# Kernel optimization log

Hardware: AMD Instinct MI355X
Metric: run time of the kernel (lower is better)

## Reference

```python
import jax, jax.numpy as jnp
import numpy as np

SENSORS = 50000
X_DIM = 64
HID = 64
Y_DIM = 32
N_EDGES = 800000


def setup_inputs() -> dict:
    key = jax.random.key(0)
    k0, k1, k2, k3 = jax.random.split(key, 4)
    x_input = jax.random.normal(k0, (1, X_DIM, SENSORS), dtype=jnp.float32)
    edge_index = jax.random.randint(k1, (2, N_EDGES), 0, SENSORS, dtype=jnp.int32)
    # GCNConv parameters (glorot-ish scaling)
    W1 = jax.random.normal(k2, (X_DIM, HID), dtype=jnp.float32) / np.sqrt(X_DIM)
    b1 = jnp.zeros((HID,), dtype=jnp.float32)
    W2 = jax.random.normal(k3, (HID, Y_DIM), dtype=jnp.float32) / np.sqrt(HID)
    b2 = jnp.zeros((Y_DIM,), dtype=jnp.float32)
    return {"x_input": x_input, "W1": W1, "b1": b1, "W2": W2, "b2": b2,
            "edge_index": edge_index}


def _gcn_conv(x, W, b, src, dst, n_nodes):
    """PyG GCNConv: x' = D^{-1/2}(A+I)D^{-1/2} (x W) + b."""
    h = x @ W  # [N, F_out]
    loop = jnp.arange(n_nodes, dtype=src.dtype)
    s = jnp.concatenate([src, loop])  # add self-loops
    d = jnp.concatenate([dst, loop])
    deg = jax.ops.segment_sum(jnp.ones_like(d, dtype=h.dtype), d,
                              num_segments=n_nodes)
    dinv = jnp.where(deg > 0, jax.lax.rsqrt(deg), 0.0)
    norm = dinv[s] * dinv[d]  # [E+N]
    msg = h[s] * norm[:, None]  # gather source features, scale
    out = jax.ops.segment_sum(msg, d, num_segments=n_nodes)  # scatter-add to targets
    return out + b


def reference(x_input, W1, b1, W2, b2, edge_index):
    B = x_input.shape[0]
    # [B, x, S] -> [B, S, x] -> [B*S, x]
    h = jnp.transpose(x_input, (0, 2, 1)).reshape(-1, X_DIM)
    n_nodes = h.shape[0]
    src, dst = edge_index[0], edge_index[1]
    h = _gcn_conv(h, W1, b1, src, dst, n_nodes)
    h = jax.nn.relu(h)
    h = _gcn_conv(h, W2, b2, src, dst, n_nodes)
    # [B*S, y] -> [B, S, y] -> [B, y, S]
    return jnp.transpose(h.reshape(B, SENSORS, Y_DIM), (0, 2, 1))
```

## Files before the change

kernel.cpp:

```cpp
#include <hip/hip_runtime.h>

#define NS 50000
#define NE 800000
#define XD 64
#define HD 64
#define YD 32

#define SHIFT 7
#define BNODES 128
#define NBUCK 391
#define BCAP 2560
#define NBLKA 256
#define EPB (NE / NBLKA)
#define SCAP 32

__device__ __forceinline__ unsigned f2b(float f) {
    union { float f; unsigned u; } c; c.f = f;
    return (c.u + 0x7fffu + ((c.u >> 16) & 1u)) >> 16;
}
__device__ __forceinline__ float blo(unsigned u) {
    union { unsigned u; float f; } c; c.u = u << 16; return c.f;
}
__device__ __forceinline__ float bhi(unsigned u) {
    union { unsigned u; float f; } c; c.u = u & 0xffff0000u; return c.f;
}

__global__ __launch_bounds__(256) void k_bucket(const int* __restrict__ src,
                                                const int* __restrict__ dst,
                                                int* __restrict__ cnt2,
                                                unsigned* __restrict__ ebuf2) {
    __shared__ unsigned se[EPB];
    __shared__ unsigned short lp[EPB];
    __shared__ int hist[NBUCK];
    int t = threadIdx.x, blk = blockIdx.x;
    int lo = blk * EPB;
    for (int i = t; i < NBUCK; i += 256) hist[i] = 0;
    __syncthreads();
    for (int i = t; i < EPB; i += 256) {
        unsigned d = (unsigned)__builtin_nontemporal_load(dst + lo + i);
        unsigned s = (unsigned)__builtin_nontemporal_load(src + lo + i);
        se[i] = (d << 16) | s;
        lp[i] = (unsigned short)atomicAdd(&hist[d >> SHIFT], 1);
    }
    __syncthreads();
    for (int i = t; i < NBUCK; i += 256)
        cnt2[blk * NBUCK + i] = min(hist[i], SCAP);
    for (int i = t; i < EPB; i += 256) {
        unsigned p = se[i];
        int b = p >> (16 + SHIFT);
        int pos = lp[i];
        if (pos < SCAP)
            ebuf2[((size_t)b * NBLKA + blk) * SCAP + pos] = p;
    }
}

__global__ __launch_bounds__(256) void k_sortxw1(const unsigned* __restrict__ ebuf2,
                                                 const int* __restrict__ cnt2,
                                                 unsigned short* __restrict__ csr,
                                                 int* __restrict__ beg,
                                                 int* __restrict__ endp,
                                                 float* __restrict__ dinv,
                                                 const float* __restrict__ x,
                                                 const float* __restrict__ W1,
                                                 unsigned* __restrict__ G1h) {
    __shared__ float w1[XD * HD];
    __shared__ unsigned se[BCAP];
    __shared__ unsigned short lcsr[BCAP];
    __shared__ int cnt[BNODES];
    __shared__ int offl[BNODES];
    __shared__ int cur[BNODES];
    __shared__ int sm[256];
    __shared__ int wsum[4];
    int b = blockIdx.x, t = threadIdx.x;
    int lane = t & 63, w = t >> 6;
    for (int i = t; i < XD * HD; i += 256) w1[i] = W1[i];
    int c = cnt2[t * NBUCK + b];
    int v = c;
#pragma unroll
    for (int d = 1; d < 64; d <<= 1) {
        int o = __shfl_up(v, d);
        if (lane >= d) v += o;
    }
    if (lane == 63) wsum[w] = v;
    if (t < BNODES) cnt[t] = 0;
    __syncthreads();
    int wpre = 0;
#pragma unroll
    for (int i = 0; i < 4; ++i) wpre += (i < w) ? wsum[i] : 0;
    int soff = wpre + v - c;
    int ntot = wsum[0] + wsum[1] + wsum[2] + wsum[3];
    int n = min(ntot, BCAP);
    {
        const unsigned* sb = ebuf2 + ((size_t)b * NBLKA + t) * SCAP;
        for (int j = 0; j < c; j += 4) {
            uint4 vv = *(const uint4*)&sb[j];
            int p = soff + j;
            if (p < BCAP) se[p] = vv.x;
            if (j + 1 < c && p + 1 < BCAP) se[p + 1] = vv.y;
            if (j + 2 < c && p + 2 < BCAP) se[p + 2] = vv.z;
            if (j + 3 < c && p + 3 < BCAP) se[p + 3] = vv.w;
        }
    }
    __syncthreads();
    for (int i = t; i < n; i += 256) atomicAdd(&cnt[(se[i] >> 16) & (BNODES - 1)], 1);
    __syncthreads();
    int v2 = (t < BNODES) ? cnt[t] : 0;
    sm[t] = v2;
    __syncthreads();
    int val2 = v2;
    for (int o = 1; o < BNODES; o <<= 1) {
        int other = (t >= o) ? sm[t - o] : 0;
        __syncthreads();
        val2 += other;
        sm[t] = val2;
        __syncthreads();
    }
    if (t < BNODES) { offl[t] = val2 - v2; cur[t] = val2 - v2; }
    __syncthreads();
    for (int i = t; i < n; i += 256) {
        unsigned p = se[i];
        int l = (p >> 16) & (BNODES - 1);
        int pos = atomicAdd(&cur[l], 1);
        lcsr[pos] = (unsigned short)(p & 0xffffu);
    }
    __syncthreads();
    unsigned* gc = (unsigned*)(csr + (size_t)b * BCAP);
    int nw = (n + 1) >> 1;
    for (int i = t; i < nw; i += 256) gc[i] = ((const unsigned*)lcsr)[i];
    if (t < BNODES) {
        int node = b * BNODES + t;
        if (node < NS) {
            int bg = b * BCAP + offl[t];
            beg[node] = bg;
            endp[node] = bg + cnt[t];
            dinv[node] = rsqrtf((float)cnt[t] + 1.0f);
        }
    }
    int half = t >> 7, tn = t & (BNODES - 1);
    int node = b * BNODES + tn;
    if (node >= NS) return;
    float4 acc[8];
#pragma unroll
    for (int i = 0; i < 8; ++i) acc[i] = make_float4(0.f, 0.f, 0.f, 0.f);
    for (int xf = 0; xf < XD; ++xf) {
        float xv = __builtin_nontemporal_load(&x[(size_t)xf * NS + node]);
        const float4* wr = (const float4*)&w1[xf * HD + half * 32];
#pragma unroll
        for (int i = 0; i < 8; ++i) {
            float4 wv = wr[i];
            acc[i].x += xv * wv.x; acc[i].y += xv * wv.y;
            acc[i].z += xv * wv.z; acc[i].w += xv * wv.w;
        }
    }
    float dv = rsqrtf((float)cnt[tn] + 1.0f);
    unsigned pk[16];
#pragma unroll
    for (int i = 0; i < 8; ++i) {
        pk[2 * i]     = f2b(dv * acc[i].x) | (f2b(dv * acc[i].y) << 16);
        pk[2 * i + 1] = f2b(dv * acc[i].z) | (f2b(dv * acc[i].w) << 16);
    }
    uint4* o = (uint4*)&G1h[(size_t)node * 32 + half * 16];
#pragma unroll
    for (int i = 0; i < 4; ++i) o[i] = ((uint4*)pk)[i];
}

__global__ __launch_bounds__(256) void k_g1l2(const int* __restrict__ beg,
                                              const int* __restrict__ endp,
                                              const unsigned short* __restrict__ csr,
                                              const unsigned* __restrict__ G1h,
                                              const float* __restrict__ dinv,
                                              const float* __restrict__ b1,
                                              const float* __restrict__ W2,
                                              unsigned* __restrict__ G2h) {
    __shared__ float w2s[HD * YD];
    __shared__ float bsh[HD];
    __shared__ float lds_h[16][68];
    __shared__ float lds_dv[16];
    int t = threadIdx.x;
    for (int i = t; i < HD * YD; i += 256) w2s[i] = W2[i];
    if (t < HD) bsh[t] = b1[t];
    __syncthreads();

    int nl = t >> 4;
    int l  = t & 15;
    int node = blockIdx.x * 16 + nl;
    int beg_ = beg[node], end_ = endp[node];
    float a0 = 0.f, a1 = 0.f, a2 = 0.f, a3 = 0.f;
#pragma unroll 4
    for (int e = beg_; e < end_; ++e) {
        int s = (int)csr[e];
        uint2 u = *(const uint2*)&G1h[(unsigned)s * 32u + 2u * l];
        a0 += blo(u.x); a1 += bhi(u.x);
        a2 += blo(u.y); a3 += bhi(u.y);
    }
    uint2 us = *(const uint2*)&G1h[(unsigned)node * 32u + 2u * l];
    float dv = dinv[node];
    float4 h;
    h.x = fmaxf(fmaf(dv, a0 + blo(us.x), bsh[4 * l + 0]), 0.f);
    h.y = fmaxf(fmaf(dv, a1 + bhi(us.x), bsh[4 * l + 1]), 0.f);
    h.z = fmaxf(fmaf(dv, a2 + blo(us.y), bsh[4 * l + 2]), 0.f);
    h.w = fmaxf(fmaf(dv, a3 + bhi(us.y), bsh[4 * l + 3]), 0.f);
    *(float4*)&lds_h[nl][4 * l] = h;
    if (l == 0) lds_dv[nl] = dv;
    __syncthreads();

    int n2 = t >> 4;
    int oo = (t & 15) * 2;
    float dv2 = lds_dv[n2];
    const float* hr = &lds_h[n2][0];
    float p0 = 0.f, p1 = 0.f;
#pragma unroll
    for (int f4 = 0; f4 < 16; ++f4) {
        float4 hv = *(const float4*)&hr[f4 * 4];
        float2 wa = *(const float2*)&w2s[(f4 * 4 + 0) * YD + oo];
        float2 wb = *(const float2*)&w2s[(f4 * 4 + 1) * YD + oo];
        float2 wc = *(const float2*)&w2s[(f4 * 4 + 2) * YD + oo];
        float2 wd = *(const float2*)&w2s[(f4 * 4 + 3) * YD + oo];
        p0 = fmaf(hv.x, wa.x, p0); p1 = fmaf(hv.x, wa.y, p1);
        p0 = fmaf(hv.y, wb.x, p0); p1 = fmaf(hv.y, wb.y, p1);
        p0 = fmaf(hv.z, wc.x, p0); p1 = fmaf(hv.z, wc.y, p1);
        p0 = fmaf(hv.w, wd.x, p0); p1 = fmaf(hv.w, wd.y, p1);
    }
    int node2 = blockIdx.x * 16 + n2;
    G2h[(size_t)node2 * 16 + (t & 15)] = f2b(dv2 * p0) | (f2b(dv2 * p1) << 16);
}

__global__ __launch_bounds__(256) void k_g2out(const int* __restrict__ beg,
                                               const int* __restrict__ endp,
                                               const unsigned short* __restrict__ csr,
                                               const unsigned* __restrict__ G2h,
                                               const float* __restrict__ dinv,
                                               const float* __restrict__ b2,
                                               float* __restrict__ out) {
    __shared__ float ot[32][33];
    __shared__ float b2s[YD];
    int t = threadIdx.x;
    if (t < YD) b2s[t] = b2[t];
    int g = t >> 3;
    int l = t & 7;
    int base_n = blockIdx.x * 32;
    int node = base_n + g;
    if (node < NS) {
        int beg_ = beg[node], end_ = endp[node];
        float a0 = 0.f, a1 = 0.f, a2 = 0.f, a3 = 0.f;
#pragma unroll 4
        for (int e = beg_; e < end_; ++e) {
            int s = (int)csr[e];
            uint2 u = *(const uint2*)&G2h[(unsigned)s * 16u + 2u * l];
            a0 += blo(u.x); a1 += bhi(u.x);
            a2 += blo(u.y); a3 += bhi(u.y);
        }
        uint2 us = *(const uint2*)&G2h[(unsigned)node * 16u + 2u * l];
        float dv = dinv[node];
        ot[g][4 * l + 0] = dv * (a0 + blo(us.x));
        ot[g][4 * l + 1] = dv * (a1 + bhi(us.x));
        ot[g][4 * l + 2] = dv * (a2 + blo(us.y));
        ot[g][4 * l + 3] = dv * (a3 + bhi(us.y));
    }
    __syncthreads();
#pragma unroll
    for (int k = 0; k < 4; ++k) {
        int idx = k * 256 + t;
        int o = idx >> 5, n = idx & 31;
        int nd = base_n + n;
        if (nd < NS)
            out[(size_t)o * NS + nd] = ot[n][o] + b2s[o];
    }
}

extern "C" void kernel_launch(void* const* d_in, const int* in_sizes, int n_in,
                              void* d_out, int out_size, void* d_ws, size_t ws_size,
                              hipStream_t stream) {
    const float* x  = (const float*)d_in[0];
    const float* W1 = (const float*)d_in[1];
    const float* b1 = (const float*)d_in[2];
    const float* W2 = (const float*)d_in[3];
    const float* b2 = (const float*)d_in[4];
    const int* ei   = (const int*)d_in[5];
    const int* src = ei;
    const int* dst = ei + NE;

    int* cnt2      = (int*)d_ws;
    unsigned* ebuf2 = (unsigned*)(cnt2 + NBLKA * NBUCK);
    unsigned short* csr = (unsigned short*)(ebuf2 + (size_t)NBUCK * NBLKA * SCAP);
    int* beg      = (int*)((unsigned*)csr + (size_t)NBUCK * BCAP / 2);
    int* endp     = beg + 50000;
    float* dinv   = (float*)(endp + 50000);
    unsigned* G1h = (unsigned*)(dinv + 50000);
    unsigned* G2h = G1h + (size_t)50000 * 32;
    float* out    = (float*)d_out;

    k_bucket<<<NBLKA, 256, 0, stream>>>(src, dst, cnt2, ebuf2);
    k_sortxw1<<<NBUCK, 256, 0, stream>>>(ebuf2, cnt2, csr, beg, endp, dinv, x, W1, G1h);
    k_g1l2<<<NS / 16, 256, 0, stream>>>(beg, endp, csr, G1h, dinv, b1, W2, G2h);
    k_g2out<<<(NS + 31) / 32, 256, 0, stream>>>(beg, endp, csr, G2h, dinv, b2, out);
}
```

Baseline: 84.40 us.

## Restructure layer-2 gather as one wavefront per node with in-wave matvec

The fused layer-1 aggregation plus W2 projection kernel now assigns a whole 64-lane wavefront to each node, processed sequentially over four nodes per wave. Each lane gathers one bf16 feature per edge, and the 64x32 matvec is split across the two wave halves and combined with a shuffle. The block-wide barrier between gather and matvec is gone, and the per-lane work is simpler. In exchange, each edge load becomes a 2-byte access, nodes within a wave are serialised, and the code relies on wave-level LDS visibility through __threadfence_block.

New measurement: 99.50 us. +17.9%, slower.

```diff
diff --git a/kernel.cpp b/kernel.cpp
--- a/kernel.cpp
+++ b/kernel.cpp
@@ -23,6 +23,9 @@
 }
 __device__ __forceinline__ float bhi(unsigned u) {
     union { unsigned u; float f; } c; c.u = u & 0xffff0000u; return c.f;
+}
+__device__ __forceinline__ float u2f(unsigned short u) {
+    union { unsigned u; float f; } c; c.u = ((unsigned)u) << 16; return c.f;
 }
 
 __global__ __launch_bounds__(256) void k_bucket(const int* __restrict__ src,
@@ -174,55 +177,41 @@
                                               unsigned* __restrict__ G2h) {
     __shared__ float w2s[HD * YD];
     __shared__ float bsh[HD];
-    __shared__ float lds_h[16][68];
-    __shared__ float lds_dv[16];
+    __shared__ float hrow[4][HD + 4];
     int t = threadIdx.x;
     for (int i = t; i < HD * YD; i += 256) w2s[i] = W2[i];
     if (t < HD) bsh[t] = b1[t];
     __syncthreads();
-
-    int nl = t >> 4;
-    int l  = t & 15;
-    int node = blockIdx.x * 16 + nl;
-    int beg_ = beg[node], end_ = endp[node];
-    float a0 = 0.f, a1 = 0.f, a2 = 0.f, a3 = 0.f;
+    int wv = t >> 6, lane = t & 63;
+    const unsigned short* G1u = (const unsigned short*)G1h;
+    int o = lane & 31, hf = lane >> 5;
+#pragma unroll
+    for (int i = 0; i < 4; ++i) {
+        int node = blockIdx.x * 16 + wv * 4 + i;
+        int beg_ = beg[node], end_ = endp[node];
+        float a = 0.f;
 #pragma unroll 4
-    for (int e = beg_; e < end_; ++e) {
-        int s = (int)csr[e];
-        uint2 u = *(const uint2*)&G1h[(unsigned)s * 32u + 2u * l];
-        a0 += blo(u.x); a1 += bhi(u.x);
-        a2 += blo(u.y); a3 += bhi(u.y);
-    }
-    uint2 us = *(const uint2*)&G1h[(unsigned)node * 32u + 2u * l];
-    float dv = dinv[node];
-    float4 h;
-    h.x = fmaxf(fmaf(dv, a0 + blo(us.x), bsh[4 * l + 0]), 0.f);
-    h.y = fmaxf(fmaf(dv, a1 + bhi(us.x), bsh[4 * l + 1]), 0.f);
-    h.z = fmaxf(fmaf(dv, a2 + blo(us.y), bsh[4 * l + 2]), 0.f);
-    h.w = fmaxf(fmaf(dv, a3 + bhi(us.y), bsh[4 * l + 3]), 0.f);
-    *(float4*)&lds_h[nl][4 * l] = h;
-    if (l == 0) lds_dv[nl] = dv;
-    __syncthreads();
-
-    int n2 = t >> 4;
-    int oo = (t & 15) * 2;
-    float dv2 = lds_dv[n2];
-    const float* hr = &lds_h[n2][0];
-    float p0 = 0.f, p1 = 0.f;
-#pragma unroll
-    for (int f4 = 0; f4 < 16; ++f4) {
-        float4 hv = *(const float4*)&hr[f4 * 4];
-        float2 wa = *(const float2*)&w2s[(f4 * 4 + 0) * YD + oo];
-        float2 wb = *(const float2*)&w2s[(f4 * 4 + 1) * YD + oo];
-        float2 wc = *(const float2*)&w2s[(f4 * 4 + 2) * YD + oo];
-        float2 wd = *(const float2*)&w2s[(f4 * 4 + 3) * YD + oo];
-        p0 = fmaf(hv.x, wa.x, p0); p1 = fmaf(hv.x, wa.y, p1);
-        p0 = fmaf(hv.y, wb.x, p0); p1 = fmaf(hv.y, wb.y, p1);
-        p0 = fmaf(hv.z, wc.x, p0); p1 = fmaf(hv.z, wc.y, p1);
-        p0 = fmaf(hv.w, wd.x, p0); p1 = fmaf(hv.w, wd.y, p1);
-    }
-    int node2 = blockIdx.x * 16 + n2;
-    G2h[(size_t)node2 * 16 + (t & 15)] = f2b(dv2 * p0) | (f2b(dv2 * p1) << 16);
+        for (int e = beg_; e < end_; ++e) {
+            int s = (int)csr[e];
+            a += u2f(G1u[(unsigned)s * 64u + lane]);
+        }
+        float dv = dinv[node];
+        float h = fmaxf(fmaf(dv, a + u2f(G1u[(unsigned)node * 64u + lane]),
+                             bsh[lane]), 0.f);
+        hrow[wv][lane] = h;
+        __threadfence_block();
+        float p = 0.f;
+        const float* hr = &hrow[wv][hf * 32];
+#pragma unroll
+        for (int f = 0; f < 32; ++f)
+            p = fmaf(hr[f], w2s[(hf * 32 + f) * YD + o], p);
+        p += __shfl_xor(p, 32);
+        p *= dv;
+        float pn = __shfl_xor(p, 1);
+        if (hf == 0 && (o & 1) == 0)
+            G2h[(size_t)node * 16 + (o >> 1)] = f2b(p) | (f2b(pn) << 16);
+        __threadfence_block();
+    }
 }
 
 __global__ __launch_bounds__(256) void k_g2out(const int* __restrict__ beg,
```
